# Performance work log

Hardware: AMD Instinct MI355X
Metric: run time of the kernel (lower is better)

## Reference

```python
import jax, jax.numpy as jnp
import numpy as np

ALPHA = 0.2  # LeakyReLU negative slope
NEG_INF = -9e15


def setup_inputs() -> dict:
    key = jax.random.key(0)
    k1, k2, k3, k4 = jax.random.split(key, 4)
    B, N, Fin, Fout = 8, 2048, 128, 64
    inp = jax.random.normal(k1, (B, N, Fin), dtype=jnp.float32)
    # sparse-ish binary adjacency (avg degree ~32)
    adj = (jax.random.uniform(k2, (B, N, N)) < (32.0 / N)).astype(jnp.int32)
    # xavier_uniform with gain=1.414
    limW = 1.414 * np.sqrt(6.0 / (Fin + Fout))
    W = jax.random.uniform(k3, (Fin, Fout), minval=-limW, maxval=limW, dtype=jnp.float32)
    lima = 1.414 * np.sqrt(6.0 / (2 * Fout + 1))
    a = jax.random.uniform(k4, (2 * Fout, 1), minval=-lima, maxval=lima, dtype=jnp.float32)
    return {"input": inp, "adj": adj, "W": W, "a": a}


def reference(input, adj, W, a):
    # h: [B, N, Fout]
    h = jnp.matmul(input, W)
    Fout = W.shape[1]
    a1 = a[:Fout, 0]   # coefficient on h_i (row)
    a2 = a[Fout:, 0]   # coefficient on h_j (col)
    f1 = jnp.einsum('bnf,f->bn', h, a1)  # [B, N]
    f2 = jnp.einsum('bnf,f->bn', h, a2)  # [B, N]
    # e[b,i,j] = LeakyReLU(a1.h_i + a2.h_j) -- no [B,N,N,2F] intermediate
    e = jax.nn.leaky_relu(f1[:, :, None] + f2[:, None, :], negative_slope=ALPHA)
    attn = jnp.where(adj > 0, e, NEG_INF)
    # NOTE: original softmax over dim=1 (normalizes over source rows i for each column j)
    attn = jax.nn.softmax(attn, axis=1)
    # dropout p=0.0 (eval reference) -> identity
    h_prime = jnp.matmul(attn, h)  # [B, N, Fout]
    return jax.nn.elu(h_prime)     # concat=True path
```

## Files before the change

### kernel.cpp

```cpp
#include <hip/hip_runtime.h>
#include <math.h>

#define BB 8
#define NN 2048
#define ROWS (BB * NN)
#define FIN 128
#define FOUT 64
#define GAT_ALPHA 0.2f
#define CAP 128

__device__ __forceinline__ float lrelu(float x) { return x > 0.f ? x : GAT_ALPHA * x; }

__global__ __launch_bounds__(256) void k1_gemm(
        const float* __restrict__ inp, const float* __restrict__ W,
        const float* __restrict__ a, float* __restrict__ h,
        float* __restrict__ f1, float* __restrict__ f2,
        float* __restrict__ colsum, float* __restrict__ emptysum) {
    const int tid  = blockIdx.x * 256 + threadIdx.x;
    const int lane = threadIdx.x & 63;
    const int w    = tid >> 6;
    if (tid < ROWS) colsum[tid] = 0.f;
    if (tid < BB * FOUT) emptysum[tid] = 0.f;

    const float* i0 = inp + (size_t)w * FIN;
    const float* i1 = i0 + (size_t)4096 * FIN;
    const float* i2 = i0 + (size_t)8192 * FIN;
    const float* i3 = i0 + (size_t)12288 * FIN;
    float c0 = 0.f, c1 = 0.f, c2 = 0.f, c3 = 0.f;
    #pragma unroll 8
    for (int k = 0; k < FIN; ++k) {
        float wk = W[k * FOUT + lane];
        c0 = fmaf(i0[k], wk, c0);
        c1 = fmaf(i1[k], wk, c1);
        c2 = fmaf(i2[k], wk, c2);
        c3 = fmaf(i3[k], wk, c3);
    }
    h[(size_t)w * FOUT + lane]           = c0;
    h[((size_t)w + 4096) * FOUT + lane]  = c1;
    h[((size_t)w + 8192) * FOUT + lane]  = c2;
    h[((size_t)w + 12288) * FOUT + lane] = c3;

    float aa = a[lane], ab = a[FOUT + lane];
    float p0 = c0 * aa, q0 = c0 * ab, p1 = c1 * aa, q1 = c1 * ab;
    float p2 = c2 * aa, q2 = c2 * ab, p3 = c3 * aa, q3 = c3 * ab;
    #pragma unroll
    for (int off = 32; off; off >>= 1) {
        p0 += __shfl_xor(p0, off, 64); q0 += __shfl_xor(q0, off, 64);
        p1 += __shfl_xor(p1, off, 64); q1 += __shfl_xor(q1, off, 64);
        p2 += __shfl_xor(p2, off, 64); q2 += __shfl_xor(q2, off, 64);
        p3 += __shfl_xor(p3, off, 64); q3 += __shfl_xor(q3, off, 64);
    }
    if (lane == 0) {
        f1[w] = p0;          f2[w] = q0;
        f1[w + 4096] = p1;   f2[w + 4096] = q1;
        f1[w + 8192] = p2;   f2[w + 8192] = q2;
        f1[w + 12288] = p3;  f2[w + 12288] = q3;
    }
}

__global__ __launch_bounds__(256) void k2_scan(
        const int* __restrict__ adj, const float* __restrict__ f1,
        const float* __restrict__ f2, unsigned short* __restrict__ lists,
        int* __restrict__ rowcnt, float* __restrict__ colsum) {
    const int gtid = blockIdx.x * 256 + threadIdx.x;
    const int row  = gtid >> 6;
    const int lane = threadIdx.x & 63;
    const int b    = row >> 11;
    const float f1i = f1[row];
    const int4* a4 = (const int4*)(adj + (size_t)row * NN);
    const float* f2b = f2 + (b << 11);
    float* csb = colsum + (b << 11);
    unsigned short* lr = lists + (size_t)row * CAP;

    int4 v0 = a4[lane];       int4 v1 = a4[64 + lane];
    int4 v2 = a4[128 + lane]; int4 v3 = a4[192 + lane];
    int4 v4 = a4[256 + lane]; int4 v5 = a4[320 + lane];
    int4 v6 = a4[384 + lane]; int4 v7 = a4[448 + lane];

    unsigned mask = 0u;
    #define ACCM(v, base) \
        mask |= ((v.x != 0) ? 1u : 0u) << (base); \
        mask |= ((v.y != 0) ? 1u : 0u) << ((base) + 1); \
        mask |= ((v.z != 0) ? 1u : 0u) << ((base) + 2); \
        mask |= ((v.w != 0) ? 1u : 0u) << ((base) + 3);
    ACCM(v0, 0)  ACCM(v1, 4)  ACCM(v2, 8)  ACCM(v3, 12)
    ACCM(v4, 16) ACCM(v5, 20) ACCM(v6, 24) ACCM(v7, 28)
    #undef ACCM

    int my = __popc(mask);
    int sc = my;
    #pragma unroll
    for (int off = 1; off < 64; off <<= 1) {
        int n = __shfl_up(sc, off, 64);
        if (lane >= off) sc += n;
    }
    int pos = sc - my;
    unsigned m = mask;
    while (m) {
        int t = __ffs(m) - 1; m &= m - 1;
        int j = ((t >> 2) << 8) + (lane << 2) + (t & 3);
        if (pos < CAP) lr[pos] = (unsigned short)j;
        atomicAdd(&csb[j], expf(lrelu(f1i + f2b[j])));
        ++pos;
    }
    if (lane == 63) rowcnt[row] = min(sc, CAP);
}

__global__ __launch_bounds__(256) void k3b_empty(
        const float* __restrict__ colsum, const float* __restrict__ h,
        float* __restrict__ emptysum) {
    int c = blockIdx.x * 256 + threadIdx.x;
    if (c >= ROWS) return;
    if (colsum[c] == 0.f) {
        int b = c >> 11;
        const float* hr = h + (size_t)c * FOUT;
        for (int f = 0; f < FOUT; ++f)
            atomicAdd(&emptysum[b * FOUT + f], hr[f] * (1.0f / NN));
    }
}

__global__ __launch_bounds__(256) void k4_out(
        const unsigned short* __restrict__ lists, const int* __restrict__ rowcnt,
        const float* __restrict__ f1, const float* __restrict__ f2,
        const float* __restrict__ colsum, const float* __restrict__ h,
        const float* __restrict__ emptysum, float* __restrict__ out) {
    const int gtid = blockIdx.x * 256 + threadIdx.x;
    const int row  = gtid >> 6;
    const int lane = threadIdx.x & 63;
    const int b    = row >> 11;
    const int cnt  = rowcnt[row];
    const float f1i = f1[row];
    const unsigned short* lr = lists + (size_t)row * CAP;
    const float* f2b = f2 + (b << 11);
    const float* csb = colsum + (b << 11);
    const float* hb  = h + ((size_t)(b << 11)) * FOUT;

    int   j_lo = 0; float w_lo = 0.f;
    if (lane < cnt) {
        j_lo = lr[lane];
        w_lo = expf(lrelu(f1i + f2b[j_lo])) / csb[j_lo];
    }
    int   j_hi = 0; float w_hi = 0.f;
    if (cnt > 64 && lane + 64 < cnt) {
        j_hi = lr[lane + 64];
        w_hi = expf(lrelu(f1i + f2b[j_hi])) / csb[j_hi];
    }

    const int c4 = (cnt + 3) & ~3;
    float a0 = 0.f, a1 = 0.f, a2 = 0.f, a3 = 0.f;
    const int lo = c4 < 64 ? c4 : 64;
    for (int t = 0; t < lo; t += 4) {
        int   j0 = __shfl(j_lo, t, 64),     j1 = __shfl(j_lo, t + 1, 64);
        int   j2 = __shfl(j_lo, t + 2, 64), j3 = __shfl(j_lo, t + 3, 64);
        float w0 = __shfl(w_lo, t, 64),     w1 = __shfl(w_lo, t + 1, 64);
        float w2 = __shfl(w_lo, t + 2, 64), w3 = __shfl(w_lo, t + 3, 64);
        a0 = fmaf(w0, hb[(size_t)j0 * FOUT + lane], a0);
        a1 = fmaf(w1, hb[(size_t)j1 * FOUT + lane], a1);
        a2 = fmaf(w2, hb[(size_t)j2 * FOUT + lane], a2);
        a3 = fmaf(w3, hb[(size_t)j3 * FOUT + lane], a3);
    }
    if (c4 > 64) {
        for (int t = 64; t < c4; t += 4) {
            int   j0 = __shfl(j_hi, t - 64, 64), j1 = __shfl(j_hi, t - 63, 64);
            int   j2 = __shfl(j_hi, t - 62, 64), j3 = __shfl(j_hi, t - 61, 64);
            float w0 = __shfl(w_hi, t - 64, 64), w1 = __shfl(w_hi, t - 63, 64);
            float w2 = __shfl(w_hi, t - 62, 64), w3 = __shfl(w_hi, t - 61, 64);
            a0 = fmaf(w0, hb[(size_t)j0 * FOUT + lane], a0);
            a1 = fmaf(w1, hb[(size_t)j1 * FOUT + lane], a1);
            a2 = fmaf(w2, hb[(size_t)j2 * FOUT + lane], a2);
            a3 = fmaf(w3, hb[(size_t)j3 * FOUT + lane], a3);
        }
    }
    float acc = ((a0 + a1) + (a2 + a3)) + emptysum[b * FOUT + lane];
    out[(size_t)row * FOUT + lane] = acc > 0.f ? acc : expm1f(acc);
}

extern "C" void kernel_launch(void* const* d_in, const int* in_sizes, int n_in,
                              void* d_out, int out_size, void* d_ws, size_t ws_size,
                              hipStream_t stream) {
    const float* inp = (const float*)d_in[0];
    const int*   adj = (const int*)d_in[1];
    const float* W   = (const float*)d_in[2];
    const float* a   = (const float*)d_in[3];
    float* out = (float*)d_out;

    char* ws = (char*)d_ws;
    float*          h        = (float*)(ws);
    unsigned short* lists    = (unsigned short*)(ws + 4194304);
    float*          f1       = (float*)(ws + 8388608);
    float*          f2       = (float*)(ws + 8454144);
    float*          colsum   = (float*)(ws + 8519680);
    int*            rowcnt   = (int*)(ws + 8585216);
    float*          emptysum = (float*)(ws + 8650752);

    k1_gemm<<<1024, 256, 0, stream>>>(inp, W, a, h, f1, f2, colsum, emptysum);
    k2_scan<<<4096, 256, 0, stream>>>(adj, f1, f2, lists, rowcnt, colsum);
    k3b_empty<<<ROWS / 256, 256, 0, stream>>>(colsum, h, emptysum);
    k4_out<<<4096, 256, 0, stream>>>(lists, rowcnt, f1, f2, colsum, h,
                                     emptysum, out);
}
```

Before: 251.9 us.

## Vectorize GEMM loads, nontemporal adjacency loads, fast exp/rcp, wider gather unroll

The GEMM kernel now reads input rows as float4 and processes four k values per iteration. The adjacency scan uses nontemporal vector loads so the large int adjacency stream does not pollute cache. Exact expf and division are replaced by __expf and the hardware reciprocal, which is slightly less accurate. The output gather loop is unrolled to eight neighbors per step to keep more independent loads in flight.

```diff
diff --git a/kernel.cpp b/kernel.cpp
--- a/kernel.cpp
+++ b/kernel.cpp
@@ -8,6 +8,8 @@
 #define FOUT 64
 #define GAT_ALPHA 0.2f
 #define CAP 128
+
+typedef int vint4 __attribute__((ext_vector_type(4)));
 
 __device__ __forceinline__ float lrelu(float x) { return x > 0.f ? x : GAT_ALPHA * x; }
 
@@ -22,18 +24,22 @@
     if (tid < ROWS) colsum[tid] = 0.f;
     if (tid < BB * FOUT) emptysum[tid] = 0.f;
 
-    const float* i0 = inp + (size_t)w * FIN;
-    const float* i1 = i0 + (size_t)4096 * FIN;
-    const float* i2 = i0 + (size_t)8192 * FIN;
-    const float* i3 = i0 + (size_t)12288 * FIN;
+    const float4* I0 = (const float4*)(inp + (size_t)w * FIN);
+    const float4* I1 = (const float4*)(inp + ((size_t)w + 4096) * FIN);
+    const float4* I2 = (const float4*)(inp + ((size_t)w + 8192) * FIN);
+    const float4* I3 = (const float4*)(inp + ((size_t)w + 12288) * FIN);
     float c0 = 0.f, c1 = 0.f, c2 = 0.f, c3 = 0.f;
-    #pragma unroll 8
-    for (int k = 0; k < FIN; ++k) {
-        float wk = W[k * FOUT + lane];
-        c0 = fmaf(i0[k], wk, c0);
-        c1 = fmaf(i1[k], wk, c1);
-        c2 = fmaf(i2[k], wk, c2);
-        c3 = fmaf(i3[k], wk, c3);
+    #pragma unroll 4
+    for (int q = 0; q < FIN / 4; ++q) {
+        float4 x0 = I0[q], x1 = I1[q], x2 = I2[q], x3 = I3[q];
+        float w0 = W[(q * 4 + 0) * FOUT + lane];
+        float w1 = W[(q * 4 + 1) * FOUT + lane];
+        float w2 = W[(q * 4 + 2) * FOUT + lane];
+        float w3 = W[(q * 4 + 3) * FOUT + lane];
+        c0 = fmaf(x0.x, w0, fmaf(x0.y, w1, fmaf(x0.z, w2, fmaf(x0.w, w3, c0))));
+        c1 = fmaf(x1.x, w0, fmaf(x1.y, w1, fmaf(x1.z, w2, fmaf(x1.w, w3, c1))));
+        c2 = fmaf(x2.x, w0, fmaf(x2.y, w1, fmaf(x2.z, w2, fmaf(x2.w, w3, c2))));
+        c3 = fmaf(x3.x, w0, fmaf(x3.y, w1, fmaf(x3.z, w2, fmaf(x3.w, w3, c3))));
     }
     h[(size_t)w * FOUT + lane]           = c0;
     h[((size_t)w + 4096) * FOUT + lane]  = c1;
@@ -67,15 +73,19 @@
     const int lane = threadIdx.x & 63;
     const int b    = row >> 11;
     const float f1i = f1[row];
-    const int4* a4 = (const int4*)(adj + (size_t)row * NN);
+    const vint4* a4 = (const vint4*)(adj + (size_t)row * NN);
     const float* f2b = f2 + (b << 11);
     float* csb = colsum + (b << 11);
     unsigned short* lr = lists + (size_t)row * CAP;
 
-    int4 v0 = a4[lane];       int4 v1 = a4[64 + lane];
-    int4 v2 = a4[128 + lane]; int4 v3 = a4[192 + lane];
-    int4 v4 = a4[256 + lane]; int4 v5 = a4[320 + lane];
-    int4 v6 = a4[384 + lane]; int4 v7 = a4[448 + lane];
+    vint4 v0 = __builtin_nontemporal_load(a4 + lane);
+    vint4 v1 = __builtin_nontemporal_load(a4 + 64 + lane);
+    vint4 v2 = __builtin_nontemporal_load(a4 + 128 + lane);
+    vint4 v3 = __builtin_nontemporal_load(a4 + 192 + lane);
+    vint4 v4 = __builtin_nontemporal_load(a4 + 256 + lane);
+    vint4 v5 = __builtin_nontemporal_load(a4 + 320 + lane);
+    vint4 v6 = __builtin_nontemporal_load(a4 + 384 + lane);
+    vint4 v7 = __builtin_nontemporal_load(a4 + 448 + lane);
 
     unsigned mask = 0u;
     #define ACCM(v, base) \
@@ -100,7 +110,7 @@
         int t = __ffs(m) - 1; m &= m - 1;
         int j = ((t >> 2) << 8) + (lane << 2) + (t & 3);
         if (pos < CAP) lr[pos] = (unsigned short)j;
-        atomicAdd(&csb[j], expf(lrelu(f1i + f2b[j])));
+        atomicAdd(&csb[j], __expf(lrelu(f1i + f2b[j])));
         ++pos;
     }
     if (lane == 63) rowcnt[row] = min(sc, CAP);
@@ -138,37 +148,49 @@
     int   j_lo = 0; float w_lo = 0.f;
     if (lane < cnt) {
         j_lo = lr[lane];
-        w_lo = expf(lrelu(f1i + f2b[j_lo])) / csb[j_lo];
+        w_lo = __expf(lrelu(f1i + f2b[j_lo])) * __builtin_amdgcn_rcpf(csb[j_lo]);
     }
     int   j_hi = 0; float w_hi = 0.f;
     if (cnt > 64 && lane + 64 < cnt) {
         j_hi = lr[lane + 64];
-        w_hi = expf(lrelu(f1i + f2b[j_hi])) / csb[j_hi];
-    }
-
-    const int c4 = (cnt + 3) & ~3;
+        w_hi = __expf(lrelu(f1i + f2b[j_hi])) * __builtin_amdgcn_rcpf(csb[j_hi]);
+    }
+
     float a0 = 0.f, a1 = 0.f, a2 = 0.f, a3 = 0.f;
-    const int lo = c4 < 64 ? c4 : 64;
-    for (int t = 0; t < lo; t += 4) {
-        int   j0 = __shfl(j_lo, t, 64),     j1 = __shfl(j_lo, t + 1, 64);
-        int   j2 = __shfl(j_lo, t + 2, 64), j3 = __shfl(j_lo, t + 3, 64);
-        float w0 = __shfl(w_lo, t, 64),     w1 = __shfl(w_lo, t + 1, 64);
-        float w2 = __shfl(w_lo, t + 2, 64), w3 = __shfl(w_lo, t + 3, 64);
-        a0 = fmaf(w0, hb[(size_t)j0 * FOUT + lane], a0);
-        a1 = fmaf(w1, hb[(size_t)j1 * FOUT + lane], a1);
-        a2 = fmaf(w2, hb[(size_t)j2 * FOUT + lane], a2);
-        a3 = fmaf(w3, hb[(size_t)j3 * FOUT + lane], a3);
-    }
-    if (c4 > 64) {
-        for (int t = 64; t < c4; t += 4) {
-            int   j0 = __shfl(j_hi, t - 64, 64), j1 = __shfl(j_hi, t - 63, 64);
-            int   j2 = __shfl(j_hi, t - 62, 64), j3 = __shfl(j_hi, t - 61, 64);
-            float w0 = __shfl(w_hi, t - 64, 64), w1 = __shfl(w_hi, t - 63, 64);
-            float w2 = __shfl(w_hi, t - 62, 64), w3 = __shfl(w_hi, t - 61, 64);
-            a0 = fmaf(w0, hb[(size_t)j0 * FOUT + lane], a0);
-            a1 = fmaf(w1, hb[(size_t)j1 * FOUT + lane], a1);
-            a2 = fmaf(w2, hb[(size_t)j2 * FOUT + lane], a2);
-            a3 = fmaf(w3, hb[(size_t)j3 * FOUT + lane], a3);
+    {
+        const int c8 = cnt >= 64 ? 64 : ((cnt + 7) & ~7);
+        for (int t = 0; t < c8; t += 8) {
+            int   j0 = __shfl(j_lo, t, 64),     j1 = __shfl(j_lo, t + 1, 64);
+            int   j2 = __shfl(j_lo, t + 2, 64), j3 = __shfl(j_lo, t + 3, 64);
+            int   j4 = __shfl(j_lo, t + 4, 64), j5 = __shfl(j_lo, t + 5, 64);
+            int   j6 = __shfl(j_lo, t + 6, 64), j7 = __shfl(j_lo, t + 7, 64);
+            float w0 = __shfl(w_lo, t, 64),     w1 = __shfl(w_lo, t + 1, 64);
+            float w2 = __shfl(w_lo, t + 2, 64), w3 = __shfl(w_lo, t + 3, 64);
+            float w4 = __shfl(w_lo, t + 4, 64), w5 = __shfl(w_lo, t + 5, 64);
+            float w6 = __shfl(w_lo, t + 6, 64), w7 = __shfl(w_lo, t + 7, 64);
+            float h0 = hb[(size_t)j0 * FOUT + lane];
+            float h1 = hb[(size_t)j1 * FOUT + lane];
+            float h2 = hb[(size_t)j2 * FOUT + lane];
+            float h3 = hb[(size_t)j3 * FOUT + lane];
+            float h4 = hb[(size_t)j4 * FOUT + lane];
+            float h5 = hb[(size_t)j5 * FOUT + lane];
+            float h6 = hb[(size_t)j6 * FOUT + lane];
+            float h7 = hb[(size_t)j7 * FOUT + lane];
+            a0 = fmaf(w0, h0, a0); a1 = fmaf(w1, h1, a1);
+            a2 = fmaf(w2, h2, a2); a3 = fmaf(w3, h3, a3);
+            a0 = fmaf(w4, h4, a0); a1 = fmaf(w5, h5, a1);
+            a2 = fmaf(w6, h6, a2); a3 = fmaf(w7, h7, a3);
+        }
+    }
+    if (cnt > 64) {
+        const int c8h = ((cnt - 64) + 7) & ~7;
+        for (int t = 0; t < c8h; t += 8) {
+            #pragma unroll
+            for (int i = 0; i < 8; ++i) {
+                int   jj = __shfl(j_hi, t + i, 64);
+                float ww = __shfl(w_hi, t + i, 64);
+                a0 = fmaf(ww, hb[(size_t)jj * FOUT + lane], a0);
+            }
         }
     }
     float acc = ((a0 + a1) + (a2 + a3)) + emptysum[b * FOUT + lane];
```

New measurement: 263.2 us. 1.04x slower.
